# Performance work log

Hardware: AMD Instinct MI355X
Metric: run time of the kernel (lower is better)

## Reference

```python
import jax, jax.numpy as jnp
import numpy as np

H = 16  # num_heads
NEG = -1.0e9


def setup_inputs() -> dict:
    key = jax.random.key(0)
    ks = jax.random.split(key, 12)
    B, Q, D, S = 2, 2048, 1024, 512
    sc = 0.02
    return {
        "main_input": jax.random.normal(ks[0], (B, Q, D), jnp.float32),
        "side_input": jax.random.normal(ks[1], (S, D), jnp.float32),
        "att_mask": jax.random.randint(ks[2], (B, Q, Q + S), 0, 2, jnp.int32),
        "Wq": jax.random.normal(ks[3], (D, D), jnp.float32) * sc,
        "bq": jnp.zeros((D,), jnp.float32),
        "Wk": jax.random.normal(ks[4], (D, D), jnp.float32) * sc,
        "bk": jnp.zeros((D,), jnp.float32),
        "Wv": jax.random.normal(ks[5], (D, D), jnp.float32) * sc,
        "bv": jnp.zeros((D,), jnp.float32),
        "Wo": jax.random.normal(ks[6], (D, D), jnp.float32) * sc,
        "bo": jnp.zeros((D,), jnp.float32),
    }


def _heads(x, W, b):
    # x: [..., D] -> [..., H, d]
    y = x @ W + b
    return y.reshape(y.shape[:-1] + (H, y.shape[-1] // H))


def reference(main_input, side_input, att_mask, Wq, bq, Wk, bk, Wv, bv, Wo, bo):
    B, Q, D = main_input.shape
    S = side_input.shape[0]
    d = D // H
    q = _heads(main_input, Wq, bq)          # [B,Q,H,d]
    k = _heads(main_input, Wk, bk)          # [B,Q,H,d]
    v = _heads(main_input, Wv, bv)          # [B,Q,H,d]
    sk = _heads(side_input, Wk, bk)         # [S,H,d] (shared projections)
    sv = _heads(side_input, Wv, bv)         # [S,H,d]
    scores_main = jnp.einsum('bqhd,bkhd->bhqk', q, k)
    scores_side = jnp.einsum('bqhd,khd->bhqk', q, sk)
    scores = jnp.concatenate([scores_main, scores_side], axis=3)  # [B,H,Q,Q+S]
    scores = scores / jnp.sqrt(jnp.asarray(d, scores.dtype))
    adder = NEG * (1.0 - att_mask.astype(scores.dtype))[:, None, :, :]
    probs = jax.nn.softmax(scores + adder, axis=-1)
    out_main = jnp.einsum('bhqk,bkhd->bqhd', probs[..., :Q], v)
    out_side = jnp.einsum('bhqk,khd->bqhd', probs[..., Q:], sv)
    att = (out_main + out_side).reshape(B, Q, D)
    return att @ Wo + bo
```

## Files before the change

### kernel.cpp

```cpp
#include <hip/hip_runtime.h>
#include <cstdint>

typedef short s16x8 __attribute__((ext_vector_type(8)));
typedef short s16x4 __attribute__((ext_vector_type(4)));
typedef unsigned short u16x4 __attribute__((ext_vector_type(4)));
typedef float f32x4 __attribute__((ext_vector_type(4)));
typedef float f32x16 __attribute__((ext_vector_type(16)));
typedef unsigned int u32x4 __attribute__((ext_vector_type(4)));

#define ND 1024
#define NH 16
#define DH 64
#define NQ 2048
#define NL 2560
#define MMAIN 4096
#define MCAT 4608
#define Q_SCALE 0.18033688011112042f

__device__ __forceinline__ unsigned short f2b(float f) {
  unsigned u = __builtin_bit_cast(unsigned, f);
  u += 0x7FFFu + ((u >> 16) & 1u);
  return (unsigned short)(u >> 16);
}

__device__ __forceinline__ void gload16(const void* g, void* l) {
  __builtin_amdgcn_global_load_lds(
      (const __attribute__((address_space(1))) void*)(unsigned long long)(uintptr_t)g,
      (__attribute__((address_space(3))) void*)(unsigned)(uintptr_t)l,
      16, 0, 0);
}

__device__ __forceinline__ f32x4 mfma16(s16x8 a, s16x8 b, f32x4 c) {
  return __builtin_amdgcn_mfma_f32_16x16x32_bf16(a, b, c, 0, 0, 0);
}
__device__ __forceinline__ f32x16 mfma32(s16x8 a, s16x8 b, f32x16 c) {
  return __builtin_amdgcn_mfma_f32_32x32x16_bf16(a, b, c, 0, 0, 0);
}

__device__ __forceinline__ float exp2g(float x) {
#if __has_builtin(__builtin_amdgcn_exp2f)
  return __builtin_amdgcn_exp2f(x);
#else
  return exp2f(x);
#endif
}

__device__ __forceinline__ int sext_bit(unsigned w, int c) {
#if __has_builtin(__builtin_amdgcn_sbfe)
  return __builtin_amdgcn_sbfe((int)w, c, 1);
#else
  return -(int)((w >> c) & 1u);
#endif
}

__device__ __forceinline__ unsigned cvt_pk_bf16(float lo, float hi) {
  unsigned d;
  asm("v_cvt_pk_bf16_f32 %0, %1, %2" : "=v"(d) : "v"(lo), "v"(hi));
  return d;
}

__device__ __forceinline__ void plane32_swap(unsigned& a, unsigned& b) {
  asm("v_permlane32_swap_b32 %0, %1" : "+v"(a), "+v"(b));
}

__device__ __forceinline__ f32x16 z16() {
  f32x16 v;
#pragma unroll
  for (int i = 0; i < 16; ++i) v[i] = 0.f;
  return v;
}


__global__ __launch_bounds__(256) void k_convert_x(const float* __restrict__ mainp,
                                                   const float* __restrict__ sidep,
                                                   short* __restrict__ xcat) {
  size_t i4 = ((size_t)blockIdx.x * 256 + threadIdx.x) * 4;
  const float* src = (i4 < (size_t)MMAIN * ND) ? (mainp + i4) : (sidep + (i4 - (size_t)MMAIN * ND));
  float4 v = *(const float4*)src;
  s16x4 o;
  o[0] = (short)f2b(v.x); o[1] = (short)f2b(v.y);
  o[2] = (short)f2b(v.z); o[3] = (short)f2b(v.w);
  *(s16x4*)(xcat + i4) = o;
}

__global__ __launch_bounds__(256) void k_transpose_w(const float* __restrict__ W0,
                                                     const float* __restrict__ W1,
                                                     const float* __restrict__ W2,
                                                     const float* __restrict__ W3,
                                                     short* __restrict__ Wt) {
  __shared__ float T[64][65];
  const float* W = blockIdx.z == 0 ? W0 : blockIdx.z == 1 ? W1 : blockIdx.z == 2 ? W2 : W3;
  short* out = Wt + (size_t)blockIdx.z * (ND * ND);
  const int tid = threadIdx.x;
  const int r = tid >> 2, c0 = (tid & 3) * 16;
  const int k0 = blockIdx.x * 64, n0 = blockIdx.y * 64;
#pragma unroll
  for (int i = 0; i < 4; ++i) {
    float4 v = *(const float4*)(W + (size_t)(k0 + r) * ND + n0 + c0 + i * 4);
    T[r][c0 + i * 4 + 0] = v.x; T[r][c0 + i * 4 + 1] = v.y;
    T[r][c0 + i * 4 + 2] = v.z; T[r][c0 + i * 4 + 3] = v.w;
  }
  __syncthreads();
  s16x8 o0, o1;
#pragma unroll
  for (int i = 0; i < 8; ++i) o0[i] = (short)f2b(T[c0 + i][r]);
#pragma unroll
  for (int i = 0; i < 8; ++i) o1[i] = (short)f2b(T[c0 + 8 + i][r]);
  *(s16x8*)(out + (size_t)(n0 + r) * ND + k0 + c0) = o0;
  *(s16x8*)(out + (size_t)(n0 + r) * ND + k0 + c0 + 8) = o1;
}

__global__ __launch_bounds__(256) void k_pack_mask(const int* __restrict__ mask,
                                                   unsigned* __restrict__ pm) {
  int W = blockIdx.x * 256 + threadIdx.x;
  const int4* src = (const int4*)(mask + (size_t)W * 32);
  unsigned bits = 0;
#pragma unroll
  for (int i = 0; i < 8; ++i) {
    int4 v = src[i];
    bits |= (unsigned)(v.x & 1) << (i * 4 + 0);
    bits |= (unsigned)(v.y & 1) << (i * 4 + 1);
    bits |= (unsigned)(v.z & 1) << (i * 4 + 2);
    bits |= (unsigned)(v.w & 1) << (i * 4 + 3);
  }
  pm[W] = bits;
}


__global__ __launch_bounds__(256) void k_gemm_qkv(const short* __restrict__ A,
                                                  const short* __restrict__ Bt,
                                                  const float* __restrict__ bqp,
                                                  const float* __restrict__ bkp,
                                                  const float* __restrict__ bvp,
                                                  short* __restrict__ qb,
                                                  short* __restrict__ kb,
                                                  short* __restrict__ vt) {
  __shared__ __align__(16) short As[128 * 64];
  __shared__ __align__(16) short Bs[128 * 64];
  const int tid = threadIdx.x;
  const int w = tid >> 6, l = tid & 63;
  const int lg = l >> 4, li = l & 15;
  const int wr = w >> 1, wc = w & 1;
  const int fid = blockIdx.x + 24 * blockIdx.y;
  const int rid = (fid & 7) * 108 + (fid >> 3);
  const int m0 = (rid / 24) * 128, n0 = (rid % 24) * 128;

  f32x4 acc[4][4];
#pragma unroll
  for (int i = 0; i < 4; ++i)
#pragma unroll
    for (int j = 0; j < 4; ++j) acc[i][j] = (f32x4){0.f, 0.f, 0.f, 0.f};

  const int cb = (l & 7) ^ (l >> 3);
  const int rsub = l >> 3;

  for (int kt = 0; kt < 16; ++kt) {
    __syncthreads();
#pragma unroll
    for (int i = 0; i < 4; ++i) {
      int c = w * 4 + i;
      int rr = c * 8 + rsub;
      gload16(A + (size_t)(m0 + rr) * ND + kt * 64 + cb * 8, As + c * 512);
      gload16(Bt + (size_t)(n0 + rr) * ND + kt * 64 + cb * 8, Bs + c * 512);
    }
    __syncthreads();
#pragma unroll
    for (int kk = 0; kk < 2; ++kk) {
      const int blk = (((kk * 4) + lg) ^ (l & 7)) * 8;
      s16x8 af[4], bf[4];
#pragma unroll
      for (int mf = 0; mf < 4; ++mf)
        af[mf] = *(const s16x8*)(As + (wr * 64 + mf * 16 + li) * 64 + blk);
#pragma unroll
      for (int nf = 0; nf < 4; ++nf)
        bf[nf] = *(const s16x8*)(Bs + (wc * 64 + nf * 16 + li) * 64 + blk);
#pragma unroll
      for (int mf = 0; mf < 4; ++mf)
#pragma unroll
        for (int nf = 0; nf < 4; ++nf)
          acc[mf][nf] = mfma16(af[mf], bf[nf], acc[mf][nf]);
    }
  }

#pragma unroll
  for (int mf = 0; mf < 4; ++mf) {
#pragma unroll
    for (int nf = 0; nf < 4; ++nf) {
      const int n = n0 + wc * 64 + nf * 16 + li;
      const int proj = n >> 10, nn = n & 1023;
      const int h = nn >> 6, dd = nn & 63;
      const float bn = (proj == 0 ? bqp : proj == 1 ? bkp : bvp)[nn];
      const int mbase = m0 + wr * 64 + mf * 16 + lg * 4;
      if (proj == 0) {
        if (mbase < MMAIN) {
#pragma unroll
          for (int r = 0; r < 4; ++r) {
            int m = mbase + r;
            int b = m >> 11, q = m & 2047;
            qb[((size_t)(b * NH + h) * NQ + q) * DH + dd] =
                (short)f2b((acc[mf][nf][r] + bn) * Q_SCALE);
          }
        }
      } else if (proj == 1) {
#pragma unroll
        for (int r = 0; r < 4; ++r) {
          int m = mbase + r;
          short v = (short)f2b(acc[mf][nf][r] + bn);
          if (m < MMAIN) {
            int b = m >> 11, p = m & 2047;
            kb[((size_t)(b * NH + h) * NL + p) * DH + dd] = v;
          } else {
            int p = NQ + (m - MMAIN);
            kb[((size_t)h * NL + p) * DH + dd] = v;
            kb[((size_t)(NH + h) * NL + p) * DH + dd] = v;
          }
        }
      } else {
        u16x4 vv;
#pragma unroll
        for (int r = 0; r < 4; ++r) vv[r] = f2b(acc[mf][nf][r] + bn);
        if (mbase < MMAIN) {
          int b = mbase >> 11, p = mbase & 2047;
          *(u16x4*)(vt + ((size_t)(b * NH + h) * DH + dd) * NL + p) = vv;
        } else {
          int p = NQ + (mbase - MMAIN);
          *(u16x4*)(vt + ((size_t)h * DH + dd) * NL + p) = vv;
          *(u16x4*)(vt + ((size_t)(NH + h) * DH + dd) * NL + p) = vv;
        }
      }
    }
  }
}


__global__ __launch_bounds__(256) void k_gemm_out(const short* __restrict__ A,
                                                  const short* __restrict__ Bt,
                                                  const float* __restrict__ bias,
                                                  float* __restrict__ outp) {
  __shared__ __align__(16) short As[128 * 64];
  __shared__ __align__(16) short Bs[128 * 64];
  const int tid = threadIdx.x;
  const int w = tid >> 6, l = tid & 63;
  const int lg = l >> 4, li = l & 15;
  const int wr = w >> 1, wc = w & 1;
  const int fid = blockIdx.x + 8 * blockIdx.y;
  const int rid = (fid & 7) * 32 + (fid >> 3);
  const int m0 = (rid / 8) * 128, n0 = (rid % 8) * 128;

  f32x4 acc[4][4];
#pragma unroll
  for (int i = 0; i < 4; ++i)
#pragma unroll
    for (int j = 0; j < 4; ++j) acc[i][j] = (f32x4){0.f, 0.f, 0.f, 0.f};

  const int cb = (l & 7) ^ (l >> 3);
  const int rsub = l >> 3;

  for (int kt = 0; kt < 16; ++kt) {
    __syncthreads();
#pragma unroll
    for (int i = 0; i < 4; ++i) {
      int c = w * 4 + i;
      int rr = c * 8 + rsub;
      gload16(A + (size_t)(m0 + rr) * ND + kt * 64 + cb * 8, As + c * 512);
      gload16(Bt + (size_t)(n0 + rr) * ND + kt * 64 + cb * 8, Bs + c * 512);
    }
    __syncthreads();
#pragma unroll
    for (int kk = 0; kk < 2; ++kk) {
      const int blk = (((kk * 4) + lg) ^ (l & 7)) * 8;
      s16x8 af[4], bf[4];
#pragma unroll
      for (int mf = 0; mf < 4; ++mf)
        af[mf] = *(const s16x8*)(As + (wr * 64 + mf * 16 + li) * 64 + blk);
#pragma unroll
      for (int nf = 0; nf < 4; ++nf)
        bf[nf] = *(const s16x8*)(Bs + (wc * 64 + nf * 16 + li) * 64 + blk);
#pragma unroll
      for (int mf = 0; mf < 4; ++mf)
#pragma unroll
        for (int nf = 0; nf < 4; ++nf)
          acc[mf][nf] = mfma16(af[mf], bf[nf], acc[mf][nf]);
    }
  }

#pragma unroll
  for (int mf = 0; mf < 4; ++mf) {
#pragma unroll
    for (int nf = 0; nf < 4; ++nf) {
      const int n = n0 + wc * 64 + nf * 16 + li;
      const float bn = bias[n];
      const int mbase = m0 + wr * 64 + mf * 16 + lg * 4;
#pragma unroll
      for (int r = 0; r < 4; ++r)
        outp[(size_t)(mbase + r) * ND + n] = acc[mf][nf][r] + bn;
    }
  }
}


#define PROC_TILE(STV, WSV, PB0, PB1)                                        \
  do {                                                                       \
    unsigned pk_[8];                                                         \
    _Pragma("unroll") for (int r_ = 0; r_ < 16; ++r_) {                      \
      const int c_ = (r_ & 3) + 8 * (r_ >> 2);                               \
      float p_ = exp2g(STV[r_]);                                             \
      p_ = __builtin_bit_cast(float, __builtin_bit_cast(unsigned, p_) &      \
                                         (unsigned)sext_bit(WSV, c_));       \
      lr += p_;                                                              \
      STV[r_] = p_;                                                          \
    }                                                                        \
    _Pragma("unroll") for (int m_ = 0; m_ < 8; ++m_)                         \
        pk_[m_] = cvt_pk_bf16(STV[2 * m_], STV[2 * m_ + 1]);                 \
    plane32_swap(pk_[0], pk_[2]);                                            \
    plane32_swap(pk_[1], pk_[3]);                                            \
    plane32_swap(pk_[4], pk_[6]);                                            \
    plane32_swap(pk_[5], pk_[7]);                                            \
    {                                                                        \
      u32x4 t_ = {pk_[0], pk_[1], pk_[2], pk_[3]};                           \
      PB0 = __builtin_bit_cast(s16x8, t_);                                   \
    }                                                                        \
    {                                                                        \
      u32x4 t_ = {pk_[4], pk_[5], pk_[6], pk_[7]};                           \
      PB1 = __builtin_bit_cast(s16x8, t_);                                   \
    }                                                                        \
  } while (0)

#define ATTN_TILE(CUR, T, DONEXT)                                            \
  do {                                                                       \
    unsigned mw_ = pmrow[(T)];                                               \
    if (DONEXT) {                                                            \
      gload16(kg + (size_t)((T) + 1) * 2048, kl + ((CUR) ^ 1) * 4096);       \
      gload16(vg + ((T) + 1) * 32, vl + ((CUR) ^ 1) * 4096);                 \
    }                                                                        \
    f32x16 st_;                                                              \
    __builtin_amdgcn_s_setprio(1);                                           \
    st_ = mfma32(*(const s16x8*)(ldsg + (CUR) * 4096 + koff[0]), qa[0], ZACC); \
    st_ = mfma32(*(const s16x8*)(ldsg + (CUR) * 4096 + koff[1]), qa[1], st_);  \
    st_ = mfma32(*(const s16x8*)(ldsg + (CUR) * 4096 + koff[2]), qa[2], st_);  \
    st_ = mfma32(*(const s16x8*)(ldsg + (CUR) * 4096 + koff[3]), qa[3], st_);  \
    __builtin_amdgcn_s_setprio(0);                                           \
    unsigned ws_ = mw_ >> (hi * 4);                                          \
    s16x8 pb0_, pb1_;                                                        \
    PROC_TILE(st_, ws_, pb0_, pb1_);                                         \
    __builtin_amdgcn_s_setprio(1);                                           \
    {                                                                        \
      s16x8 v0_ = *(const s16x8*)(ldsg + 8192 + (CUR) * 4096 + voff[0]);     \
      s16x8 v1_ =                                                            \
          *(const s16x8*)(ldsg + 8192 + (CUR) * 4096 + voff[0] + 2048);      \
      ot0 = mfma32(v0_, pb0_, ot0);                                          \
      ot1 = mfma32(v1_, pb0_, ot1);                                          \
    }                                                                        \
    {                                                                        \
      s16x8 v0_ = *(const s16x8*)(ldsg + 8192 + (CUR) * 4096 + voff[1]);     \
      s16x8 v1_ =                                                            \
          *(const s16x8*)(ldsg + 8192 + (CUR) * 4096 + voff[1] + 2048);      \
      ot0 = mfma32(v0_, pb1_, ot0);                                          \
      ot1 = mfma32(v1_, pb1_, ot1);                                          \
    }                                                                        \
    __builtin_amdgcn_s_setprio(0);                                           \
    __syncthreads();                                                         \
  } while (0)

__global__ __launch_bounds__(512)
__attribute__((amdgpu_waves_per_eu(4, 4)))
void k_attn2(const short* __restrict__ qbuf,
             const short* __restrict__ kbuf,
             const short* __restrict__ vtbuf,
             const unsigned* __restrict__ pmask,
             short* __restrict__ attbuf) {
  __shared__ __align__(16) short lds[16384];
  char* ldsb = (char*)lds;

  const int tid = threadIdx.x;
  const int w = tid >> 6, l = tid & 63;
  const int wg = w & 3, g = w >> 2;
  const int li = l & 31, hi = l >> 5;
  const int bh = blockIdx.x;
  const int b = bh >> 4, h = bh & 15;
  const int qr0 = blockIdx.y * 128 + wg * 32;
  const size_t bhs = (size_t)bh;
  char* ldsg = ldsb + g * 16384;

  s16x8 qa[4];
  {
    const short* qp = qbuf + (bhs * NQ + qr0 + li) * DH + hi * 8;
#pragma unroll
    for (int ks = 0; ks < 4; ++ks) qa[ks] = *(const s16x8*)(qp + ks * 16);
  }

  int koff[4];
#pragma unroll
  for (int ks = 0; ks < 4; ++ks)
    koff[ks] = li * 128 + ((((ks << 1) | hi) ^ (li & 7)) << 4);

  int voff[2];
#pragma unroll
  for (int ks2 = 0; ks2 < 2; ++ks2)
    voff[ks2] = li * 64 + ((((ks2 << 1) | hi) ^ ((li >> 1) & 3)) << 4);

  const short* kg = kbuf + (bhs * NL + g * 1280 + wg * 8 + (l >> 3)) * DH +
                    (((l & 7) ^ (l >> 3)) << 3);
  const short* vg = vtbuf + (bhs * DH + wg * 16 + (l >> 2)) * NL + g * 1280 +
                    (((l & 3) ^ ((l >> 3) & 3)) << 3);
  char* kl = ldsg + wg * 1024;
  char* vl = ldsg + 8192 + wg * 1024;

  const unsigned* pmrow = pmask + ((size_t)b * NQ + qr0 + li) * 80 + g * 40;

  const f32x16 ZACC = z16();
  f32x16 ot0 = z16(), ot1 = z16();
  float lr = 0.f;

  gload16(kg, kl);
  gload16(vg, vl);
  __syncthreads();

  for (int tt = 0; tt < 20; ++tt) {
    const int t0 = 2 * tt;
    ATTN_TILE(0, t0, 1);
    ATTN_TILE(1, t0 + 1, (t0 + 2 < 40));
  }

  lr += __shfl_xor(lr, 32);

  float* comb = (float*)ldsb;
  const int half = wg >> 1;
  const int slot = ((wg & 1) * 64 + l) * 33;
  float lsum = lr;
#pragma unroll
  for (int ph = 0; ph < 2; ++ph) {
    __syncthreads();
    if (g == 1 && half == ph) {
#pragma unroll
      for (int i = 0; i < 16; ++i) comb[slot + i] = ot0[i];
#pragma unroll
      for (int i = 0; i < 16; ++i) comb[slot + 16 + i] = ot1[i];
      comb[slot + 32] = lr;
    }
    __syncthreads();
    if (g == 0 && half == ph) {
#pragma unroll
      for (int i = 0; i < 16; ++i) ot0[i] += comb[slot + i];
#pragma unroll
      for (int i = 0; i < 16; ++i) ot1[i] += comb[slot + 16 + i];
      lsum += comb[slot + 32];
    }
  }
  if (g == 0) {
    const float inv = 1.0f / lsum;
    short* orow = attbuf + ((size_t)b * NQ + qr0 + li) * ND + h * 64;
#pragma unroll
    for (int gg = 0; gg < 4; ++gg) {
      u16x4 v0, v1;
#pragma unroll
      for (int r = 0; r < 4; ++r) {
        v0[r] = f2b(ot0[gg * 4 + r] * inv);
        v1[r] = f2b(ot1[gg * 4 + r] * inv);
      }
      *(u16x4*)(orow + gg * 8 + hi * 4) = v0;
      *(u16x4*)(orow + 32 + gg * 8 + hi * 4) = v1;
    }
  }
}


extern "C" void kernel_launch(void* const* d_in, const int* in_sizes, int n_in,
                              void* d_out, int out_size, void* d_ws, size_t ws_size,
                              hipStream_t stream) {
  const float* mainp = (const float*)d_in[0];
  const float* sidep = (const float*)d_in[1];
  const int* mask = (const int*)d_in[2];
  const float* Wq = (const float*)d_in[3];
  const float* bq = (const float*)d_in[4];
  const float* Wk = (const float*)d_in[5];
  const float* bk = (const float*)d_in[6];
  const float* Wv = (const float*)d_in[7];
  const float* bv = (const float*)d_in[8];
  const float* Wo = (const float*)d_in[9];
  const float* bo = (const float*)d_in[10];

  char* ws = (char*)d_ws;
  short* xcat   = (short*)(ws + 0);
  short* Wt     = (short*)(ws + 9437184);
  short* qbuf   = (short*)(ws + 17825792);
  short* kbuf   = (short*)(ws + 26214400);
  short* vtbuf  = (short*)(ws + 36700160);
  short* attbuf = (short*)(ws + 47185920);
  unsigned* pmask = (unsigned*)(ws + 55574528);

  k_convert_x<<<4608, 256, 0, stream>>>(mainp, sidep, xcat);
  k_transpose_w<<<dim3(16, 16, 4), 256, 0, stream>>>(Wq, Wk, Wv, Wo, Wt);
  k_pack_mask<<<1280, 256, 0, stream>>>(mask, pmask);

  k_gemm_qkv<<<dim3(24, 36), 256, 0, stream>>>(xcat, Wt, bq, bk, bv, qbuf, kbuf, vtbuf);

  k_attn2<<<dim3(32, 16), 512, 0, stream>>>(qbuf, kbuf, vtbuf, pmask, attbuf);

  k_gemm_out<<<dim3(8, 32), 256, 0, stream>>>(attbuf, Wt + 3145728, bo, (float*)d_out);
}
```

Before: 156.3 us.

## Merge prep kernels, narrow output GEMM tiles, use raw v_exp, relax attention occupancy

Folds the three preprocessing kernels (activation conversion, weight transpose, mask packing) into one launch selected by block index, removing two kernel launches and their gaps. The output GEMM tile shrinks from 128x128 to 128x64, doubling the grid to 512 blocks for better CU coverage at the cost of more A-tile reloads. The softmax exp2 now uses inline v_exp_f32 assembly. The attention kernel drops its fixed waves_per_eu(4,4) hint in favour of launch_bounds(512,2), which can change register allocation.

```diff
diff --git a/kernel.cpp b/kernel.cpp
--- a/kernel.cpp
+++ b/kernel.cpp
@@ -37,12 +37,10 @@
   return __builtin_amdgcn_mfma_f32_32x32x16_bf16(a, b, c, 0, 0, 0);
 }
 
-__device__ __forceinline__ float exp2g(float x) {
-#if __has_builtin(__builtin_amdgcn_exp2f)
-  return __builtin_amdgcn_exp2f(x);
-#else
-  return exp2f(x);
-#endif
+__device__ __forceinline__ float exp2r(float x) {
+  float r;
+  asm("v_exp_f32 %0, %1" : "=v"(r) : "v"(x));
+  return r;
 }
 
 __device__ __forceinline__ int sext_bit(unsigned w, int c) {
@@ -71,59 +69,63 @@
 }
 
 
-__global__ __launch_bounds__(256) void k_convert_x(const float* __restrict__ mainp,
-                                                   const float* __restrict__ sidep,
-                                                   short* __restrict__ xcat) {
-  size_t i4 = ((size_t)blockIdx.x * 256 + threadIdx.x) * 4;
-  const float* src = (i4 < (size_t)MMAIN * ND) ? (mainp + i4) : (sidep + (i4 - (size_t)MMAIN * ND));
-  float4 v = *(const float4*)src;
-  s16x4 o;
-  o[0] = (short)f2b(v.x); o[1] = (short)f2b(v.y);
-  o[2] = (short)f2b(v.z); o[3] = (short)f2b(v.w);
-  *(s16x4*)(xcat + i4) = o;
-}
-
-__global__ __launch_bounds__(256) void k_transpose_w(const float* __restrict__ W0,
-                                                     const float* __restrict__ W1,
-                                                     const float* __restrict__ W2,
-                                                     const float* __restrict__ W3,
-                                                     short* __restrict__ Wt) {
+__global__ __launch_bounds__(256) void k_prep(const float* __restrict__ mainp,
+                                              const float* __restrict__ sidep,
+                                              const int* __restrict__ mask,
+                                              const float* __restrict__ W0,
+                                              const float* __restrict__ W1,
+                                              const float* __restrict__ W2,
+                                              const float* __restrict__ W3,
+                                              short* __restrict__ xcat,
+                                              short* __restrict__ Wt,
+                                              unsigned* __restrict__ pm) {
   __shared__ float T[64][65];
-  const float* W = blockIdx.z == 0 ? W0 : blockIdx.z == 1 ? W1 : blockIdx.z == 2 ? W2 : W3;
-  short* out = Wt + (size_t)blockIdx.z * (ND * ND);
+  const int bid = blockIdx.x;
   const int tid = threadIdx.x;
-  const int r = tid >> 2, c0 = (tid & 3) * 16;
-  const int k0 = blockIdx.x * 64, n0 = blockIdx.y * 64;
-#pragma unroll
-  for (int i = 0; i < 4; ++i) {
-    float4 v = *(const float4*)(W + (size_t)(k0 + r) * ND + n0 + c0 + i * 4);
-    T[r][c0 + i * 4 + 0] = v.x; T[r][c0 + i * 4 + 1] = v.y;
-    T[r][c0 + i * 4 + 2] = v.z; T[r][c0 + i * 4 + 3] = v.w;
-  }
-  __syncthreads();
-  s16x8 o0, o1;
-#pragma unroll
-  for (int i = 0; i < 8; ++i) o0[i] = (short)f2b(T[c0 + i][r]);
-#pragma unroll
-  for (int i = 0; i < 8; ++i) o1[i] = (short)f2b(T[c0 + 8 + i][r]);
-  *(s16x8*)(out + (size_t)(n0 + r) * ND + k0 + c0) = o0;
-  *(s16x8*)(out + (size_t)(n0 + r) * ND + k0 + c0 + 8) = o1;
-}
-
-__global__ __launch_bounds__(256) void k_pack_mask(const int* __restrict__ mask,
-                                                   unsigned* __restrict__ pm) {
-  int W = blockIdx.x * 256 + threadIdx.x;
-  const int4* src = (const int4*)(mask + (size_t)W * 32);
-  unsigned bits = 0;
-#pragma unroll
-  for (int i = 0; i < 8; ++i) {
-    int4 v = src[i];
-    bits |= (unsigned)(v.x & 1) << (i * 4 + 0);
-    bits |= (unsigned)(v.y & 1) << (i * 4 + 1);
-    bits |= (unsigned)(v.z & 1) << (i * 4 + 2);
-    bits |= (unsigned)(v.w & 1) << (i * 4 + 3);
-  }
-  pm[W] = bits;
+  if (bid < 4608) {
+    size_t i4 = ((size_t)bid * 256 + tid) * 4;
+    const float* src =
+        (i4 < (size_t)MMAIN * ND) ? (mainp + i4) : (sidep + (i4 - (size_t)MMAIN * ND));
+    float4 v = *(const float4*)src;
+    s16x4 o;
+    o[0] = (short)f2b(v.x); o[1] = (short)f2b(v.y);
+    o[2] = (short)f2b(v.z); o[3] = (short)f2b(v.w);
+    *(s16x4*)(xcat + i4) = o;
+  } else if (bid < 4608 + 1024) {
+    const int id = bid - 4608;
+    const int z = id >> 8, rem = id & 255;
+    const float* W = z == 0 ? W0 : z == 1 ? W1 : z == 2 ? W2 : W3;
+    short* out = Wt + (size_t)z * (ND * ND);
+    const int r = tid >> 2, c0 = (tid & 3) * 16;
+    const int k0 = (rem & 15) * 64, n0 = (rem >> 4) * 64;
+#pragma unroll
+    for (int i = 0; i < 4; ++i) {
+      float4 v = *(const float4*)(W + (size_t)(k0 + r) * ND + n0 + c0 + i * 4);
+      T[r][c0 + i * 4 + 0] = v.x; T[r][c0 + i * 4 + 1] = v.y;
+      T[r][c0 + i * 4 + 2] = v.z; T[r][c0 + i * 4 + 3] = v.w;
+    }
+    __syncthreads();
+    s16x8 o0, o1;
+#pragma unroll
+    for (int i = 0; i < 8; ++i) o0[i] = (short)f2b(T[c0 + i][r]);
+#pragma unroll
+    for (int i = 0; i < 8; ++i) o1[i] = (short)f2b(T[c0 + 8 + i][r]);
+    *(s16x8*)(out + (size_t)(n0 + r) * ND + k0 + c0) = o0;
+    *(s16x8*)(out + (size_t)(n0 + r) * ND + k0 + c0 + 8) = o1;
+  } else {
+    const int W = (bid - 5632) * 256 + tid;
+    const int4* src = (const int4*)(mask + (size_t)W * 32);
+    unsigned bits = 0;
+#pragma unroll
+    for (int i = 0; i < 8; ++i) {
+      int4 v = src[i];
+      bits |= (unsigned)(v.x & 1) << (i * 4 + 0);
+      bits |= (unsigned)(v.y & 1) << (i * 4 + 1);
+      bits |= (unsigned)(v.z & 1) << (i * 4 + 2);
+      bits |= (unsigned)(v.w & 1) << (i * 4 + 3);
+    }
+    pm[W] = bits;
+  }
 }
 
 
@@ -238,20 +240,20 @@
                                                   const float* __restrict__ bias,
                                                   float* __restrict__ outp) {
   __shared__ __align__(16) short As[128 * 64];
-  __shared__ __align__(16) short Bs[128 * 64];
+  __shared__ __align__(16) short Bs[64 * 64];
   const int tid = threadIdx.x;
   const int w = tid >> 6, l = tid & 63;
   const int lg = l >> 4, li = l & 15;
   const int wr = w >> 1, wc = w & 1;
-  const int fid = blockIdx.x + 8 * blockIdx.y;
-  const int rid = (fid & 7) * 32 + (fid >> 3);
-  const int m0 = (rid / 8) * 128, n0 = (rid % 8) * 128;
-
-  f32x4 acc[4][4];
+  const int fid = blockIdx.x + 16 * blockIdx.y;
+  const int rid = (fid & 7) * 64 + (fid >> 3);
+  const int m0 = (rid >> 4) * 128, n0 = (rid & 15) * 64;
+
+  f32x4 acc[4][2];
 #pragma unroll
   for (int i = 0; i < 4; ++i)
 #pragma unroll
-    for (int j = 0; j < 4; ++j) acc[i][j] = (f32x4){0.f, 0.f, 0.f, 0.f};
+    for (int j = 0; j < 2; ++j) acc[i][j] = (f32x4){0.f, 0.f, 0.f, 0.f};
 
   const int cb = (l & 7) ^ (l >> 3);
   const int rsub = l >> 3;
@@ -263,23 +265,28 @@
       int c = w * 4 + i;
       int rr = c * 8 + rsub;
       gload16(A + (size_t)(m0 + rr) * ND + kt * 64 + cb * 8, As + c * 512);
+    }
+#pragma unroll
+    for (int i = 0; i < 2; ++i) {
+      int c = w * 2 + i;
+      int rr = c * 8 + rsub;
       gload16(Bt + (size_t)(n0 + rr) * ND + kt * 64 + cb * 8, Bs + c * 512);
     }
     __syncthreads();
 #pragma unroll
     for (int kk = 0; kk < 2; ++kk) {
       const int blk = (((kk * 4) + lg) ^ (l & 7)) * 8;
-      s16x8 af[4], bf[4];
+      s16x8 af[4], bf[2];
 #pragma unroll
       for (int mf = 0; mf < 4; ++mf)
         af[mf] = *(const s16x8*)(As + (wr * 64 + mf * 16 + li) * 64 + blk);
 #pragma unroll
-      for (int nf = 0; nf < 4; ++nf)
-        bf[nf] = *(const s16x8*)(Bs + (wc * 64 + nf * 16 + li) * 64 + blk);
+      for (int nf = 0; nf < 2; ++nf)
+        bf[nf] = *(const s16x8*)(Bs + (wc * 32 + nf * 16 + li) * 64 + blk);
 #pragma unroll
       for (int mf = 0; mf < 4; ++mf)
 #pragma unroll
-        for (int nf = 0; nf < 4; ++nf)
+        for (int nf = 0; nf < 2; ++nf)
           acc[mf][nf] = mfma16(af[mf], bf[nf], acc[mf][nf]);
     }
   }
@@ -287,8 +294,8 @@
 #pragma unroll
   for (int mf = 0; mf < 4; ++mf) {
 #pragma unroll
-    for (int nf = 0; nf < 4; ++nf) {
-      const int n = n0 + wc * 64 + nf * 16 + li;
+    for (int nf = 0; nf < 2; ++nf) {
+      const int n = n0 + wc * 32 + nf * 16 + li;
       const float bn = bias[n];
       const int mbase = m0 + wr * 64 + mf * 16 + lg * 4;
 #pragma unroll
@@ -304,7 +311,7 @@
     unsigned pk_[8];                                                         \
     _Pragma("unroll") for (int r_ = 0; r_ < 16; ++r_) {                      \
       const int c_ = (r_ & 3) + 8 * (r_ >> 2);                               \
-      float p_ = exp2g(STV[r_]);                                             \
+      float p_ = exp2r(STV[r_]);                                             \
       p_ = __builtin_bit_cast(float, __builtin_bit_cast(unsigned, p_) &      \
                                          (unsigned)sext_bit(WSV, c_));       \
       lr += p_;                                                              \
@@ -362,13 +369,11 @@
     __syncthreads();                                                         \
   } while (0)
 
-__global__ __launch_bounds__(512)
-__attribute__((amdgpu_waves_per_eu(4, 4)))
-void k_attn2(const short* __restrict__ qbuf,
-             const short* __restrict__ kbuf,
-             const short* __restrict__ vtbuf,
-             const unsigned* __restrict__ pmask,
-             short* __restrict__ attbuf) {
+__global__ __launch_bounds__(512, 2) void k_attn2(const short* __restrict__ qbuf,
+                                                  const short* __restrict__ kbuf,
+                                                  const short* __restrict__ vtbuf,
+                                                  const unsigned* __restrict__ pmask,
+                                                  short* __restrict__ attbuf) {
   __shared__ __align__(16) short lds[16384];
   char* ldsb = (char*)lds;
 
@@ -489,13 +494,12 @@
   short* attbuf = (short*)(ws + 47185920);
   unsigned* pmask = (unsigned*)(ws + 55574528);
 
-  k_convert_x<<<4608, 256, 0, stream>>>(mainp, sidep, xcat);
-  k_transpose_w<<<dim3(16, 16, 4), 256, 0, stream>>>(Wq, Wk, Wv, Wo, Wt);
-  k_pack_mask<<<1280, 256, 0, stream>>>(mask, pmask);
+  k_prep<<<6912, 256, 0, stream>>>(mainp, sidep, mask, Wq, Wk, Wv, Wo,
+                                   xcat, Wt, pmask);
 
   k_gemm_qkv<<<dim3(24, 36), 256, 0, stream>>>(xcat, Wt, bq, bk, bv, qbuf, kbuf, vtbuf);
 
   k_attn2<<<dim3(32, 16), 512, 0, stream>>>(qbuf, kbuf, vtbuf, pmask, attbuf);
 
-  k_gemm_out<<<dim3(8, 32), 256, 0, stream>>>(attbuf, Wt + 3145728, bo, (float*)d_out);
-}
+  k_gemm_out<<<dim3(16, 32), 256, 0, stream>>>(attbuf, Wt + 3145728, bo, (float*)d_out);
+}
```

Result: faster. 148.7 us (median of 3 runs) (-4.9%).
